# Performance work log

Hardware: AMD Instinct MI355X
Metric: run time of the kernel (lower is better)

Reference implementation:

```python
import jax, jax.numpy as jnp
import numpy as np

B, Q, T, C = 2, 300, 25, 256
NH, NL, NP = 8, 4, 4
DFF = 1024
HD = C // NH
SHAPES = [(128, 128), (64, 64), (32, 32), (16, 16)]  # (H_l, W_l) per level
S = sum(h * w for h, w in SHAPES)
LQ = Q * T


def setup_inputs() -> dict:
    key = jax.random.key(0)
    ks = jax.random.split(key, 16)
    rn = lambda k, shape, s=0.02: jax.random.normal(k, shape, jnp.float32) * s
    starts = np.cumsum([0] + [h * w for h, w in SHAPES[:-1]])
    return {
        "tgt_text": jax.random.normal(ks[0], (B, Q, T, C), jnp.float32),
        "query_pos_text": jax.random.normal(ks[1], (B, Q, T, C), jnp.float32),
        "reference_points": jax.random.uniform(ks[2], (B, LQ, NL, 2), jnp.float32),
        "src": jax.random.normal(ks[3], (B, S, C), jnp.float32),
        "src_spatial_shapes": jnp.array(SHAPES, jnp.int32),
        "level_start_index": jnp.array(starts, jnp.int32),
        "in_proj_w": rn(ks[4], (3 * C, C)), "in_proj_b": jnp.zeros((3 * C,), jnp.float32),
        "out_proj_w": rn(ks[5], (C, C)), "out_proj_b": jnp.zeros((C,), jnp.float32),
        "ln1_g": jnp.ones((C,), jnp.float32), "ln1_b": jnp.zeros((C,), jnp.float32),
        "samp_off_w": rn(ks[6], (NH * NL * NP * 2, C)), "samp_off_b": rn(ks[7], (NH * NL * NP * 2,), 0.5),
        "aw_w": rn(ks[8], (NH * NL * NP, C)), "aw_b": jnp.zeros((NH * NL * NP,), jnp.float32),
        "vp_w": rn(ks[9], (C, C)), "vp_b": jnp.zeros((C,), jnp.float32),
        "op_w": rn(ks[10], (C, C)), "op_b": jnp.zeros((C,), jnp.float32),
        "ln2_g": jnp.ones((C,), jnp.float32), "ln2_b": jnp.zeros((C,), jnp.float32),
        "ffn1_w": rn(ks[11], (DFF, C)), "ffn1_b": jnp.zeros((DFF,), jnp.float32),
        "ffn2_w": rn(ks[12], (C, DFF)), "ffn2_b": jnp.zeros((C,), jnp.float32),
        "ln3_g": jnp.ones((C,), jnp.float32), "ln3_b": jnp.zeros((C,), jnp.float32),
    }


def _ln(x, g, b):
    m = jnp.mean(x, axis=-1, keepdims=True)
    v = jnp.var(x, axis=-1, keepdims=True)
    return (x - m) / jnp.sqrt(v + 1e-5) * g + b


def _self_attn(tgt, pos, in_proj_w, in_proj_b, out_proj_w, out_proj_b):
    # torch nn.MultiheadAttention math: q,k carry pos, v is raw tgt
    qk = (tgt + pos).reshape(B * Q, T, C)
    x = tgt.reshape(B * Q, T, C)
    Wq, Wk, Wv = jnp.split(in_proj_w, 3, axis=0)
    bq, bk, bv = jnp.split(in_proj_b, 3, axis=0)
    heads = lambda t: t.reshape(B * Q, T, NH, HD).transpose(0, 2, 1, 3)
    q = heads(qk @ Wq.T + bq)
    k = heads(qk @ Wk.T + bk)
    v = heads(x @ Wv.T + bv)
    attn = jax.nn.softmax(jnp.einsum("bhqd,bhkd->bhqk", q, k) / jnp.sqrt(jnp.float32(HD)), axis=-1)
    o = jnp.einsum("bhqk,bhkd->bhqd", attn, v).transpose(0, 2, 1, 3).reshape(B * Q, T, C)
    return (o @ out_proj_w.T + out_proj_b).reshape(B, Q, T, C)


def _ms_deform_attn(query, reference_points, src, shapes, samp_off_w, samp_off_b, aw_w, aw_b, vp_w, vp_b, op_w, op_b):
    # query: [B, LQ, C]; src: [B, S, C]
    value = (src @ vp_w.T + vp_b).reshape(B, S, NH, HD)
    off = (query @ samp_off_w.T + samp_off_b).reshape(B, LQ, NH, NL, NP, 2)
    aw = jax.nn.softmax((query @ aw_w.T + aw_b).reshape(B, LQ, NH, NL * NP), axis=-1)
    aw = aw.reshape(B, LQ, NH, NL, NP)
    # normalizer is (W_l, H_l)
    norm = jnp.array([[w, h] for (h, w) in shapes], jnp.float32)
    loc = reference_points[:, :, None, :, None, :] + off / norm[None, None, None, :, None, :]
    starts = np.cumsum([0] + [h * w for h, w in shapes])
    accum = jnp.zeros((B, NH, LQ, HD), jnp.float32)
    for l, (Hl, Wl) in enumerate(shapes):
        vl = value[:, starts[l]:starts[l] + Hl * Wl].transpose(0, 2, 1, 3)  # [B,NH,HW,HD]
        # grid_sample align_corners=False pixel coords
        xl = (loc[:, :, :, l, :, 0] * Wl - 0.5).transpose(0, 2, 1, 3).reshape(B, NH, LQ * NP)
        yl = (loc[:, :, :, l, :, 1] * Hl - 0.5).transpose(0, 2, 1, 3).reshape(B, NH, LQ * NP)
        x0 = jnp.floor(xl); y0 = jnp.floor(yl)
        wx1 = xl - x0; wy1 = yl - y0
        x0i = x0.astype(jnp.int32); y0i = y0.astype(jnp.int32)
        samp = jnp.zeros((B, NH, LQ * NP, HD), jnp.float32)
        for dx, dy, w in ((0, 0, (1 - wx1) * (1 - wy1)), (1, 0, wx1 * (1 - wy1)),
                          (0, 1, (1 - wx1) * wy1), (1, 1, wx1 * wy1)):
            xi = x0i + dx; yi = y0i + dy
            valid = (xi >= 0) & (xi < Wl) & (yi >= 0) & (yi < Hl)
            lin = jnp.clip(yi, 0, Hl - 1) * Wl + jnp.clip(xi, 0, Wl - 1)
            g = jnp.take_along_axis(vl, lin[..., None], axis=2)  # [B,NH,LQ*NP,HD]
            samp = samp + g * (w * valid)[..., None]
        samp = samp.reshape(B, NH, LQ, NP, HD)
        awl = aw[:, :, :, l, :].transpose(0, 2, 1, 3)  # [B,NH,LQ,NP]
        accum = accum + jnp.sum(samp * awl[..., None], axis=3)
    out = accum.transpose(0, 2, 1, 3).reshape(B, LQ, C)
    return out @ op_w.T + op_b


def reference(tgt_text, query_pos_text, reference_points, src, src_spatial_shapes, level_start_index,
              in_proj_w, in_proj_b, out_proj_w, out_proj_b, ln1_g, ln1_b,
              samp_off_w, samp_off_b, aw_w, aw_b, vp_w, vp_b, op_w, op_b, ln2_g, ln2_b,
              ffn1_w, ffn1_b, ffn2_w, ffn2_b, ln3_g, ln3_b):
    shapes = [tuple(int(v) for v in row) for row in np.asarray(src_spatial_shapes)]  # static
    # --- intra-text self-attention ---
    tgt2 = _self_attn(tgt_text, query_pos_text, in_proj_w, in_proj_b, out_proj_w, out_proj_b)
    tgt = _ln(tgt_text + tgt2, ln1_g, ln1_b)
    # --- multi-scale deformable cross-attention ---
    query = (tgt + query_pos_text).reshape(B, LQ, C)
    cross = _ms_deform_attn(query, reference_points, src, shapes,
                            samp_off_w, samp_off_b, aw_w, aw_b, vp_w, vp_b, op_w, op_b)
    tgt = _ln(tgt + cross.reshape(B, Q, T, C), ln2_g, ln2_b)
    # --- FFN ---
    ffn = jax.nn.relu(tgt @ ffn1_w.T + ffn1_b) @ ffn2_w.T + ffn2_b
    return _ln(tgt + ffn, ln3_g, ln3_b)
```

## Files before the change

kernel.cpp:

```cpp
#include <hip/hip_runtime.h>
#include <cstddef>

#define B_ 2
#define Q_ 300
#define T_ 25
#define C_ 256
#define NH_ 8
#define NL_ 4
#define NP_ 4
#define HD_ 32
#define DFF_ 1024
#define LQ_ (Q_ * T_)
#define NTOK_ (B_ * LQ_)
#define S_ 21760
#define BS_ (B_ * S_)

typedef __bf16 bf16x8 __attribute__((ext_vector_type(8)));
typedef float floatx4 __attribute__((ext_vector_type(4)));
typedef unsigned short ushort_t;

__device__ __forceinline__ unsigned pack_bf16(float x, float y) {
    unsigned ux = __float_as_uint(x) + 0x8000u;
    unsigned uy = __float_as_uint(y) + 0x8000u;
    return (ux >> 16) | (uy & 0xFFFF0000u);
}
__device__ __forceinline__ ushort_t f2bf_s(float x) {
    return (ushort_t)((__float_as_uint(x) + 0x8000u) >> 16);
}
__device__ __forceinline__ float bf2f(ushort_t u) {
    return __uint_as_float((unsigned)u << 16);
}

#define GBN 128
#define GBK 32
#define LDA_S 40

template<int AMODE, int OUT_BF16, int GBMT>
__global__ __launch_bounds__(256) void gemm_t(
    const void* __restrict__ Av, const float* __restrict__ A2,
    const float* __restrict__ W, const float* __restrict__ W2, int N1,
    const float* __restrict__ bias, const float* __restrict__ bias2,
    void* __restrict__ Cv, long long partStride,
    int M, int N, int K, int kChunk, int ldc, int relu)
{
    constexpr int LA = GBMT / 32;
    constexpr int WM = GBMT / 2;
    constexpr int NI = WM / 16;

    __shared__ unsigned short Asl[GBMT * LDA_S];
    __shared__ unsigned short Bsl[GBN * LDA_S];

    const int m0 = blockIdx.x * GBMT;
    const int n0 = blockIdx.y * GBN;
    const int z  = blockIdx.z;
    const int kbeg = z * kChunk;
    const int kend = min(K, kbeg + kChunk);

    const int t  = threadIdx.x;
    const int wid  = t >> 6;
    const int lane = t & 63;
    const int wm = (wid >> 1) * WM;
    const int wn = (wid & 1) * 64;
    const int fm = lane & 15;
    const int fq = (lane >> 4) * 8;

    floatx4 acc[NI][4];
    #pragma unroll
    for (int i = 0; i < NI; ++i)
        #pragma unroll
        for (int j = 0; j < 4; ++j)
            acc[i][j] = (floatx4){0.f, 0.f, 0.f, 0.f};

    float4 pa[LA];
    uint2  pab[LA];
    float4 pw[4];
    const float* Af = (const float*)Av;
    const ushort_t* Ab = (const ushort_t*)Av;

    auto load_tiles = [&](int k0) {
        #pragma unroll
        for (int i = 0; i < LA; ++i) {
            int idx = t + 256 * i;
            int row = idx >> 3;
            int c4  = (idx & 7) * 4;
            int gm = m0 + row;
            if constexpr (AMODE == 2) {
                uint2 v = {0u, 0u};
                if (gm < M) v = *(const uint2*)(Ab + (size_t)gm * K + k0 + c4);
                pab[i] = v;
            } else {
                float4 v = make_float4(0.f, 0.f, 0.f, 0.f);
                if (gm < M) {
                    v = *(const float4*)(Af + (size_t)gm * K + k0 + c4);
                    if constexpr (AMODE == 1) {
                        float4 v2 = *(const float4*)(A2 + (size_t)gm * K + k0 + c4);
                        v.x += v2.x; v.y += v2.y; v.z += v2.z; v.w += v2.w;
                    }
                }
                pa[i] = v;
            }
        }
        #pragma unroll
        for (int i = 0; i < 4; ++i) {
            int idx = t + 256 * i;
            int row = idx >> 3;
            int c4  = (idx & 7) * 4;
            int gn = n0 + row;
            const float* wr;
            if (W2 && gn >= N1) wr = W2 + (size_t)(gn - N1) * K;
            else                wr = W + (size_t)gn * K;
            pw[i] = *(const float4*)(wr + k0 + c4);
        }
    };

    load_tiles(kbeg);
    for (int k0 = kbeg; k0 < kend; k0 += GBK) {
        #pragma unroll
        for (int i = 0; i < LA; ++i) {
            int idx = t + 256 * i;
            int row = idx >> 3;
            int c4  = (idx & 7) * 4;
            if constexpr (AMODE == 2) {
                *(uint2*)&Asl[row * LDA_S + c4] = pab[i];
            } else {
                uint2 p;
                p.x = pack_bf16(pa[i].x, pa[i].y);
                p.y = pack_bf16(pa[i].z, pa[i].w);
                *(uint2*)&Asl[row * LDA_S + c4] = p;
            }
        }
        #pragma unroll
        for (int i = 0; i < 4; ++i) {
            int idx = t + 256 * i;
            int row = idx >> 3;
            int c4  = (idx & 7) * 4;
            uint2 q;
            q.x = pack_bf16(pw[i].x, pw[i].y);
            q.y = pack_bf16(pw[i].z, pw[i].w);
            *(uint2*)&Bsl[row * LDA_S + c4] = q;
        }
        __syncthreads();

        if (k0 + GBK < kend) load_tiles(k0 + GBK);

        bf16x8 af[NI], bfr[4];
        #pragma unroll
        for (int i = 0; i < NI; ++i)
            af[i] = *(const bf16x8*)&Asl[(wm + i * 16 + fm) * LDA_S + fq];
        #pragma unroll
        for (int j = 0; j < 4; ++j)
            bfr[j] = *(const bf16x8*)&Bsl[(wn + j * 16 + fm) * LDA_S + fq];

        #pragma unroll
        for (int i = 0; i < NI; ++i)
            #pragma unroll
            for (int j = 0; j < 4; ++j)
                acc[i][j] = __builtin_amdgcn_mfma_f32_16x16x32_bf16(af[i], bfr[j], acc[i][j], 0, 0, 0);
        __syncthreads();
    }

    float* Cf = (float*)Cv + (long long)z * partStride;
    ushort_t* Cb = (ushort_t*)Cv;
    const int cr = (lane >> 4) * 4;
    const int cc = lane & 15;
    #pragma unroll
    for (int j = 0; j < 4; ++j) {
        int gn = n0 + wn + j * 16 + cc;
        float bia = 0.f;
        if (z == 0) bia = (bias2 && gn >= N1) ? bias2[gn - N1] : bias[gn];
        #pragma unroll
        for (int i = 0; i < NI; ++i) {
            #pragma unroll
            for (int r = 0; r < 4; ++r) {
                int gm = m0 + wm + i * 16 + cr + r;
                if (gm < M) {
                    float v = acc[i][j][r] + bia;
                    if (relu) v = fmaxf(v, 0.f);
                    if constexpr (OUT_BF16) Cb[(size_t)gm * ldc + gn] = f2bf_s(v);
                    else                    Cf[(size_t)gm * ldc + gn] = v;
                }
            }
        }
    }
}

__global__ __launch_bounds__(64) void attn_kernel(
    const ushort_t* __restrict__ qkv,
    ushort_t* __restrict__ o)
{
    int sh = blockIdx.x;
    int s = sh >> 3, h = sh & 7;
    __shared__ float qs[T_][HD_], ks[T_][HD_], vs[T_][HD_];
    int t = threadIdx.x;

    for (int idx = t; idx < T_ * HD_; idx += 64) {
        int i = idx >> 5, d = idx & 31;
        size_t base = ((size_t)(s * T_ + i)) * 768 + h * HD_ + d;
        qs[i][d] = bf2f(qkv[base]);
        ks[i][d] = bf2f(qkv[base + 256]);
        vs[i][d] = bf2f(qkv[base + 512]);
    }
    __syncthreads();

    if (t < T_) {
        float sc[T_];
        float mx = -1e30f;
        #pragma unroll
        for (int j = 0; j < T_; ++j) {
            float dot = 0.f;
            #pragma unroll
            for (int d = 0; d < HD_; ++d) dot += qs[t][d] * ks[j][d];
            sc[j] = dot * 0.17677669529663687f;
            mx = fmaxf(mx, sc[j]);
        }
        float sum = 0.f;
        #pragma unroll
        for (int j = 0; j < T_; ++j) { sc[j] = __expf(sc[j] - mx); sum += sc[j]; }
        float inv = 1.f / sum;
        float out[HD_];
        #pragma unroll
        for (int d = 0; d < HD_; ++d) out[d] = 0.f;
        for (int j = 0; j < T_; ++j) {
            float p = sc[j] * inv;
            #pragma unroll
            for (int d = 0; d < HD_; ++d) out[d] += p * vs[j][d];
        }
        size_t ob = ((size_t)(s * T_ + t)) * C_ + h * HD_;
        #pragma unroll
        for (int d = 0; d < HD_; ++d) o[ob + d] = f2bf_s(out[d]);
    }
}

__global__ __launch_bounds__(256) void ln_kernel(
    const float* __restrict__ x, const float* __restrict__ r,
    int nparts, long long rstride,
    const float* __restrict__ g, const float* __restrict__ b,
    float* __restrict__ out, const float* __restrict__ pos,
    float* __restrict__ qout)
{
    int tok = blockIdx.x;
    int t = threadIdx.x;
    size_t base = (size_t)tok * C_;
    float v = x[base + t];
    for (int p = 0; p < nparts; ++p)
        v += r[(long long)base + t + (long long)p * rstride];

    float s = v, ss = v * v;
    #pragma unroll
    for (int off = 32; off; off >>= 1) {
        s += __shfl_down(s, off);
        ss += __shfl_down(ss, off);
    }
    __shared__ float ws[4], wss[4];
    __shared__ float mean_s, rstd_s;
    int wid = t >> 6, lane = t & 63;
    if (lane == 0) { ws[wid] = s; wss[wid] = ss; }
    __syncthreads();
    if (t == 0) {
        float S = 0.f, SS = 0.f;
        #pragma unroll
        for (int i = 0; i < 4; ++i) { S += ws[i]; SS += wss[i]; }
        float m = S / 256.f;
        float var = SS / 256.f - m * m;
        mean_s = m;
        rstd_s = rsqrtf(var + 1e-5f);
    }
    __syncthreads();
    float y = (v - mean_s) * rstd_s * g[t] + b[t];
    out[base + t] = y;
    if (qout) qout[base + t] = y + pos[base + t];
}

__global__ __launch_bounds__(256) void deform_kernel(
    const ushort_t* __restrict__ value,
    const float* __restrict__ d12,
    const float* __restrict__ refpts,
    ushort_t* __restrict__ out)
{
    const int lane = threadIdx.x & 63;
    const int wave = threadIdx.x >> 6;
    const int half = lane >> 5;
    const int tok = blockIdx.x * 8 + wave * 2 + half;
    const int h  = (lane >> 2) & 7;
    const int d8 = (lane & 3) * 8;
    const int b = tok / LQ_;

    const float* awp = d12 + (size_t)tok * 384 + 256 + h * 16;
    float logit[16];
    float mx = -1e30f;
    #pragma unroll
    for (int i = 0; i < 16; ++i) { logit[i] = awp[i]; mx = fmaxf(mx, logit[i]); }
    float sum = 0.f;
    #pragma unroll
    for (int i = 0; i < 16; ++i) { logit[i] = __expf(logit[i] - mx); sum += logit[i]; }
    float inv = 1.f / sum;

    const float* offp = d12 + (size_t)tok * 384 + h * 32;
    const float* refp = refpts + (size_t)tok * (NL_ * 2);

    const int HW[4]     = {128, 64, 32, 16};
    const int starts[4] = {0, 16384, 20480, 21504};

    float accv[8];
    #pragma unroll
    for (int i = 0; i < 8; ++i) accv[i] = 0.f;

    #pragma unroll
    for (int l = 0; l < 4; ++l) {
        const int Hl = HW[l], Wl = HW[l];
        float rx = refp[l * 2 + 0], ry = refp[l * 2 + 1];
        const ushort_t* vbase = value + ((size_t)b * S_ + starts[l]) * (NH_ * HD_) + h * HD_ + d8;
        #pragma unroll
        for (int p = 0; p < 4; ++p) {
            float ox = offp[(l * 4 + p) * 2 + 0];
            float oy = offp[(l * 4 + p) * 2 + 1];
            float xl = rx * (float)Wl + ox - 0.5f;
            float yl = ry * (float)Hl + oy - 0.5f;
            float x0f = floorf(xl), y0f = floorf(yl);
            int x0 = (int)x0f, y0 = (int)y0f;
            float wx1 = xl - x0f, wy1 = yl - y0f;
            float wx0 = 1.f - wx1, wy0 = 1.f - wy1;
            float aww = logit[l * 4 + p] * inv;

            #pragma unroll
            for (int c = 0; c < 4; ++c) {
                int dx = c & 1, dy = c >> 1;
                int xi = x0 + dx, yi = y0 + dy;
                float w = (dx ? wx1 : wx0) * (dy ? wy1 : wy0);
                bool valid = (xi >= 0) & (xi < Wl) & (yi >= 0) & (yi < Hl);
                int xc = min(max(xi, 0), Wl - 1);
                int yc = min(max(yi, 0), Hl - 1);
                float wc = (valid ? w : 0.f) * aww;
                uint4 raw = *(const uint4*)(vbase + ((size_t)(yc * Wl + xc)) * (NH_ * HD_));
                accv[0] += __uint_as_float((raw.x & 0xFFFFu) << 16) * wc;
                accv[1] += __uint_as_float(raw.x & 0xFFFF0000u) * wc;
                accv[2] += __uint_as_float((raw.y & 0xFFFFu) << 16) * wc;
                accv[3] += __uint_as_float(raw.y & 0xFFFF0000u) * wc;
                accv[4] += __uint_as_float((raw.z & 0xFFFFu) << 16) * wc;
                accv[5] += __uint_as_float(raw.z & 0xFFFF0000u) * wc;
                accv[6] += __uint_as_float((raw.w & 0xFFFFu) << 16) * wc;
                accv[7] += __uint_as_float(raw.w & 0xFFFF0000u) * wc;
            }
        }
    }
    uint4 po;
    po.x = pack_bf16(accv[0], accv[1]);
    po.y = pack_bf16(accv[2], accv[3]);
    po.z = pack_bf16(accv[4], accv[5]);
    po.w = pack_bf16(accv[6], accv[7]);
    *(uint4*)(out + (size_t)tok * C_ + h * HD_ + d8) = po;
}

extern "C" void kernel_launch(void* const* d_in, const int* in_sizes, int n_in,
                              void* d_out, int out_size, void* d_ws, size_t ws_size,
                              hipStream_t stream) {
    const float* tgt_text = (const float*)d_in[0];
    const float* pos      = (const float*)d_in[1];
    const float* refpts   = (const float*)d_in[2];
    const float* src      = (const float*)d_in[3];
    const float* in_proj_w  = (const float*)d_in[6];
    const float* in_proj_b  = (const float*)d_in[7];
    const float* out_proj_w = (const float*)d_in[8];
    const float* out_proj_b = (const float*)d_in[9];
    const float* ln1_g = (const float*)d_in[10];
    const float* ln1_b = (const float*)d_in[11];
    const float* samp_off_w = (const float*)d_in[12];
    const float* samp_off_b = (const float*)d_in[13];
    const float* aw_w = (const float*)d_in[14];
    const float* aw_b = (const float*)d_in[15];
    const float* vp_w = (const float*)d_in[16];
    const float* vp_b = (const float*)d_in[17];
    const float* op_w = (const float*)d_in[18];
    const float* op_b = (const float*)d_in[19];
    const float* ln2_g = (const float*)d_in[20];
    const float* ln2_b = (const float*)d_in[21];
    const float* ffn1_w = (const float*)d_in[22];
    const float* ffn1_b = (const float*)d_in[23];
    const float* ffn2_w = (const float*)d_in[24];
    const float* ffn2_b = (const float*)d_in[25];
    const float* ln3_g = (const float*)d_in[26];
    const float* ln3_b = (const float*)d_in[27];

    const long long NC = (long long)NTOK_ * C_;
    float* ws = (float*)d_ws;
    float* A    = ws;
    float* Bq   = ws + NC;
    float* Creg = ws + 2 * NC;
    float* D12  = Creg + (long long)NTOK_ * DFF_;
    float* E    = D12 + (long long)NTOK_ * 384;
    float* F    = E + NC;

    const int MB64  = (NTOK_ + 63) / 64;
    const int MB128 = (NTOK_ + 127) / 128;
    const int MBV64 = BS_ / 64;

    gemm_t<1, 1, 64><<<dim3(MB64, 4, 1), 256, 0, stream>>>(tgt_text, pos, in_proj_w, nullptr, 0,
        in_proj_b, nullptr, Creg, 0, NTOK_, 512, 256, 256, 768, 0);
    gemm_t<0, 1, 64><<<dim3(MB64, 2, 1), 256, 0, stream>>>(tgt_text, nullptr, in_proj_w + 512 * 256, nullptr, 0,
        in_proj_b + 512, nullptr, (void*)((ushort_t*)Creg + 512), 0, NTOK_, 256, 256, 256, 768, 0);
    attn_kernel<<<B_ * Q_ * NH_, 64, 0, stream>>>((const ushort_t*)Creg, (ushort_t*)E);
    gemm_t<2, 0, 64><<<dim3(MB64, 2, 1), 256, 0, stream>>>(E, nullptr, out_proj_w, nullptr, 0,
        out_proj_b, nullptr, F, 0, NTOK_, 256, 256, 256, 256, 0);
    ln_kernel<<<NTOK_, 256, 0, stream>>>(tgt_text, F, 1, 0,
                                         ln1_g, ln1_b, A, pos, Bq);
    gemm_t<0, 1, 64><<<dim3(MBV64, 2, 1), 256, 0, stream>>>(src, nullptr, vp_w, nullptr, 0,
        vp_b, nullptr, Creg, 0, BS_, 256, 256, 256, 256, 0);
    gemm_t<0, 0, 64><<<dim3(MB64, 3, 1), 256, 0, stream>>>(Bq, nullptr, samp_off_w, aw_w, 256,
        samp_off_b, aw_b, D12, 0, NTOK_, 384, 256, 256, 384, 0);
    deform_kernel<<<NTOK_ / 8, 256, 0, stream>>>((const ushort_t*)Creg, D12, refpts, (ushort_t*)E);
    gemm_t<2, 0, 64><<<dim3(MB64, 2, 1), 256, 0, stream>>>(E, nullptr, op_w, nullptr, 0,
        op_b, nullptr, F, 0, NTOK_, 256, 256, 256, 256, 0);
    ln_kernel<<<NTOK_, 256, 0, stream>>>(A, F, 1, 0,
                                         ln2_g, ln2_b, A, nullptr, nullptr);
    gemm_t<0, 1, 128><<<dim3(MB128, 8, 1), 256, 0, stream>>>(A, nullptr, ffn1_w, nullptr, 0,
        ffn1_b, nullptr, Creg, 0, NTOK_, DFF_, 256, 256, DFF_, 1);
    gemm_t<2, 0, 64><<<dim3(MB64, 2, 2), 256, 0, stream>>>(Creg, nullptr, ffn2_w, nullptr, 0,
        ffn2_b, nullptr, E, NC, NTOK_, 256, 1024, 512, 256, 0);
    ln_kernel<<<NTOK_, 256, 0, stream>>>(A, E, 2, NC,
                                         ln3_g, ln3_b, (float*)d_out, nullptr, nullptr);
}
```

Measured before the change: 454.4 us.

## Fuse QKV and value-projection GEMMs, head-major value layout, wave-per-token LayerNorm

Merges the Q/K, V and value-projection GEMMs into one launch that writes bf16 output. The value projection is stored head-major as [B][head][S][32], so each deformable-attention bilinear gather reads a contiguous 64-byte row per pixel. LayerNorm is rewritten so each wave handles one token with float4 loads and shuffle reductions, removing shared-memory syncs. The aim is to cut launch count, improve gather locality and raise LN memory throughput, at the cost of a scattered store in the value-GEMM epilogue.

```diff
diff --git a/kernel.cpp b/kernel.cpp
--- a/kernel.cpp
+++ b/kernel.cpp
@@ -184,6 +184,138 @@
     }
 }
 
+__global__ __launch_bounds__(256) void gemm3(
+    const float* __restrict__ tgt, const float* __restrict__ pos,
+    const float* __restrict__ src,
+    const float* __restrict__ ipw, const float* __restrict__ ipb,
+    const float* __restrict__ vpw, const float* __restrict__ vpb,
+    ushort_t* __restrict__ qkv, ushort_t* __restrict__ valt)
+{
+    __shared__ unsigned short Asl[64 * LDA_S];
+    __shared__ unsigned short Bsl[GBN * LDA_S];
+
+    int g = blockIdx.x;
+    const float *A, *A2, *W, *bias;
+    int m0, n0, M, vt;
+    ushort_t* C;
+    if (g < 940)       { A = tgt; A2 = pos;     W = ipw;             bias = ipb;
+                         m0 = (g >> 2) * 64; n0 = (g & 3) * 128; M = NTOK_; vt = 0; C = qkv; }
+    else if (g < 1410) { g -= 940; A = tgt; A2 = nullptr; W = ipw + 512 * 256; bias = ipb + 512;
+                         m0 = (g >> 1) * 64; n0 = (g & 1) * 128; M = NTOK_; vt = 0; C = qkv + 512; }
+    else               { g -= 1410; A = src; A2 = nullptr; W = vpw;  bias = vpb;
+                         m0 = (g >> 1) * 64; n0 = (g & 1) * 128; M = BS_; vt = 1; C = valt; }
+    const int K = 256;
+
+    const int t  = threadIdx.x;
+    const int wid  = t >> 6;
+    const int lane = t & 63;
+    const int wm = (wid >> 1) * 32;
+    const int wn = (wid & 1) * 64;
+    const int fm = lane & 15;
+    const int fq = (lane >> 4) * 8;
+
+    floatx4 acc[2][4];
+    #pragma unroll
+    for (int i = 0; i < 2; ++i)
+        #pragma unroll
+        for (int j = 0; j < 4; ++j)
+            acc[i][j] = (floatx4){0.f, 0.f, 0.f, 0.f};
+
+    float4 pa[2], pw[4];
+    auto load_tiles = [&](int k0) {
+        #pragma unroll
+        for (int i = 0; i < 2; ++i) {
+            int idx = t + 256 * i;
+            int row = idx >> 3;
+            int c4  = (idx & 7) * 4;
+            int gm = m0 + row;
+            float4 v = make_float4(0.f, 0.f, 0.f, 0.f);
+            if (gm < M) {
+                v = *(const float4*)(A + (size_t)gm * K + k0 + c4);
+                if (A2) {
+                    float4 v2 = *(const float4*)(A2 + (size_t)gm * K + k0 + c4);
+                    v.x += v2.x; v.y += v2.y; v.z += v2.z; v.w += v2.w;
+                }
+            }
+            pa[i] = v;
+        }
+        #pragma unroll
+        for (int i = 0; i < 4; ++i) {
+            int idx = t + 256 * i;
+            int row = idx >> 3;
+            int c4  = (idx & 7) * 4;
+            pw[i] = *(const float4*)(W + (size_t)(n0 + row) * K + k0 + c4);
+        }
+    };
+
+    load_tiles(0);
+    for (int k0 = 0; k0 < K; k0 += GBK) {
+        #pragma unroll
+        for (int i = 0; i < 2; ++i) {
+            int idx = t + 256 * i;
+            int row = idx >> 3;
+            int c4  = (idx & 7) * 4;
+            uint2 p;
+            p.x = pack_bf16(pa[i].x, pa[i].y);
+            p.y = pack_bf16(pa[i].z, pa[i].w);
+            *(uint2*)&Asl[row * LDA_S + c4] = p;
+        }
+        #pragma unroll
+        for (int i = 0; i < 4; ++i) {
+            int idx = t + 256 * i;
+            int row = idx >> 3;
+            int c4  = (idx & 7) * 4;
+            uint2 q;
+            q.x = pack_bf16(pw[i].x, pw[i].y);
+            q.y = pack_bf16(pw[i].z, pw[i].w);
+            *(uint2*)&Bsl[row * LDA_S + c4] = q;
+        }
+        __syncthreads();
+
+        if (k0 + GBK < K) load_tiles(k0 + GBK);
+
+        bf16x8 af[2], bfr[4];
+        #pragma unroll
+        for (int i = 0; i < 2; ++i)
+            af[i] = *(const bf16x8*)&Asl[(wm + i * 16 + fm) * LDA_S + fq];
+        #pragma unroll
+        for (int j = 0; j < 4; ++j)
+            bfr[j] = *(const bf16x8*)&Bsl[(wn + j * 16 + fm) * LDA_S + fq];
+
+        #pragma unroll
+        for (int i = 0; i < 2; ++i)
+            #pragma unroll
+            for (int j = 0; j < 4; ++j)
+                acc[i][j] = __builtin_amdgcn_mfma_f32_16x16x32_bf16(af[i], bfr[j], acc[i][j], 0, 0, 0);
+        __syncthreads();
+    }
+
+    const int cr = (lane >> 4) * 4;
+    const int cc = lane & 15;
+    #pragma unroll
+    for (int j = 0; j < 4; ++j) {
+        int gn = n0 + wn + j * 16 + cc;
+        float bia = bias[gn];
+        #pragma unroll
+        for (int i = 0; i < 2; ++i) {
+            #pragma unroll
+            for (int r = 0; r < 4; ++r) {
+                int gm = m0 + wm + i * 16 + cr + r;
+                if (gm < M) {
+                    ushort_t o = f2bf_s(acc[i][j][r] + bia);
+                    if (vt) {
+                        int bb = gm >= S_;
+                        int s  = gm - bb * S_;
+                        C[(((size_t)(bb * 8 + (gn >> 5))) * S_ + s) * 32 + (gn & 31)] = o;
+                    } else {
+                        C[(size_t)gm * 768 + gn] = o;
+                    }
+                }
+            }
+        }
+    }
+}
+
 __global__ __launch_bounds__(64) void attn_kernel(
     const ushort_t* __restrict__ qkv,
     ushort_t* __restrict__ o)
@@ -231,44 +363,48 @@
     }
 }
 
-__global__ __launch_bounds__(256) void ln_kernel(
+__global__ __launch_bounds__(256) void ln4_kernel(
     const float* __restrict__ x, const float* __restrict__ r,
     int nparts, long long rstride,
     const float* __restrict__ g, const float* __restrict__ b,
     float* __restrict__ out, const float* __restrict__ pos,
     float* __restrict__ qout)
 {
-    int tok = blockIdx.x;
-    int t = threadIdx.x;
-    size_t base = (size_t)tok * C_;
-    float v = x[base + t];
-    for (int p = 0; p < nparts; ++p)
-        v += r[(long long)base + t + (long long)p * rstride];
-
-    float s = v, ss = v * v;
-    #pragma unroll
-    for (int off = 32; off; off >>= 1) {
-        s += __shfl_down(s, off);
-        ss += __shfl_down(ss, off);
-    }
-    __shared__ float ws[4], wss[4];
-    __shared__ float mean_s, rstd_s;
-    int wid = t >> 6, lane = t & 63;
-    if (lane == 0) { ws[wid] = s; wss[wid] = ss; }
-    __syncthreads();
-    if (t == 0) {
-        float S = 0.f, SS = 0.f;
-        #pragma unroll
-        for (int i = 0; i < 4; ++i) { S += ws[i]; SS += wss[i]; }
-        float m = S / 256.f;
-        float var = SS / 256.f - m * m;
-        mean_s = m;
-        rstd_s = rsqrtf(var + 1e-5f);
-    }
-    __syncthreads();
-    float y = (v - mean_s) * rstd_s * g[t] + b[t];
-    out[base + t] = y;
-    if (qout) qout[base + t] = y + pos[base + t];
+    const int wave = threadIdx.x >> 6;
+    const int lane = threadIdx.x & 63;
+    const int tok = blockIdx.x * 4 + wave;
+    const size_t base = (size_t)tok * C_ + lane * 4;
+
+    float4 v = *(const float4*)(x + base);
+    for (int p = 0; p < nparts; ++p) {
+        float4 rv = *(const float4*)(r + base + (long long)p * rstride);
+        v.x += rv.x; v.y += rv.y; v.z += rv.z; v.w += rv.w;
+    }
+    float s  = v.x + v.y + v.z + v.w;
+    float ss = v.x * v.x + v.y * v.y + v.z * v.z + v.w * v.w;
+    #pragma unroll
+    for (int m = 32; m; m >>= 1) {
+        s  += __shfl_xor(s, m);
+        ss += __shfl_xor(ss, m);
+    }
+    float mean = s * (1.f / 256.f);
+    float var  = ss * (1.f / 256.f) - mean * mean;
+    float rstd = rsqrtf(var + 1e-5f);
+
+    float4 gv = *(const float4*)(g + lane * 4);
+    float4 bv = *(const float4*)(b + lane * 4);
+    float4 y;
+    y.x = (v.x - mean) * rstd * gv.x + bv.x;
+    y.y = (v.y - mean) * rstd * gv.y + bv.y;
+    y.z = (v.z - mean) * rstd * gv.z + bv.z;
+    y.w = (v.w - mean) * rstd * gv.w + bv.w;
+    *(float4*)(out + base) = y;
+    if (qout) {
+        float4 pv = *(const float4*)(pos + base);
+        float4 q;
+        q.x = y.x + pv.x; q.y = y.y + pv.y; q.z = y.z + pv.z; q.w = y.w + pv.w;
+        *(float4*)(qout + base) = q;
+    }
 }
 
 __global__ __launch_bounds__(256) void deform_kernel(
@@ -309,7 +445,7 @@
     for (int l = 0; l < 4; ++l) {
         const int Hl = HW[l], Wl = HW[l];
         float rx = refp[l * 2 + 0], ry = refp[l * 2 + 1];
-        const ushort_t* vbase = value + ((size_t)b * S_ + starts[l]) * (NH_ * HD_) + h * HD_ + d8;
+        const ushort_t* vbase = value + (((size_t)(b * 8 + h)) * S_ + starts[l]) * HD_ + d8;
         #pragma unroll
         for (int p = 0; p < 4; ++p) {
             float ox = offp[(l * 4 + p) * 2 + 0];
@@ -331,7 +467,7 @@
                 int xc = min(max(xi, 0), Wl - 1);
                 int yc = min(max(yi, 0), Hl - 1);
                 float wc = (valid ? w : 0.f) * aww;
-                uint4 raw = *(const uint4*)(vbase + ((size_t)(yc * Wl + xc)) * (NH_ * HD_));
+                uint4 raw = *(const uint4*)(vbase + (size_t)(yc * Wl + xc) * HD_);
                 accv[0] += __uint_as_float((raw.x & 0xFFFFu) << 16) * wc;
                 accv[1] += __uint_as_float(raw.x & 0xFFFF0000u) * wc;
                 accv[2] += __uint_as_float((raw.y & 0xFFFFu) << 16) * wc;
@@ -390,32 +526,30 @@
     float* E    = D12 + (long long)NTOK_ * 384;
     float* F    = E + NC;
 
+    ushort_t* qkv  = (ushort_t*)Creg;
+    ushort_t* valt = (ushort_t*)Creg + (size_t)NTOK_ * 768;
+
     const int MB64  = (NTOK_ + 63) / 64;
     const int MB128 = (NTOK_ + 127) / 128;
-    const int MBV64 = BS_ / 64;
-
-    gemm_t<1, 1, 64><<<dim3(MB64, 4, 1), 256, 0, stream>>>(tgt_text, pos, in_proj_w, nullptr, 0,
-        in_proj_b, nullptr, Creg, 0, NTOK_, 512, 256, 256, 768, 0);
-    gemm_t<0, 1, 64><<<dim3(MB64, 2, 1), 256, 0, stream>>>(tgt_text, nullptr, in_proj_w + 512 * 256, nullptr, 0,
-        in_proj_b + 512, nullptr, (void*)((ushort_t*)Creg + 512), 0, NTOK_, 256, 256, 256, 768, 0);
-    attn_kernel<<<B_ * Q_ * NH_, 64, 0, stream>>>((const ushort_t*)Creg, (ushort_t*)E);
+
+    gemm3<<<2770, 256, 0, stream>>>(tgt_text, pos, src, in_proj_w, in_proj_b,
+                                    vp_w, vp_b, qkv, valt);
+    attn_kernel<<<B_ * Q_ * NH_, 64, 0, stream>>>(qkv, (ushort_t*)E);
     gemm_t<2, 0, 64><<<dim3(MB64, 2, 1), 256, 0, stream>>>(E, nullptr, out_proj_w, nullptr, 0,
         out_proj_b, nullptr, F, 0, NTOK_, 256, 256, 256, 256, 0);
-    ln_kernel<<<NTOK_, 256, 0, stream>>>(tgt_text, F, 1, 0,
-                                         ln1_g, ln1_b, A, pos, Bq);
-    gemm_t<0, 1, 64><<<dim3(MBV64, 2, 1), 256, 0, stream>>>(src, nullptr, vp_w, nullptr, 0,
-        vp_b, nullptr, Creg, 0, BS_, 256, 256, 256, 256, 0);
+    ln4_kernel<<<NTOK_ / 4, 256, 0, stream>>>(tgt_text, F, 1, 0,
+                                              ln1_g, ln1_b, A, pos, Bq);
     gemm_t<0, 0, 64><<<dim3(MB64, 3, 1), 256, 0, stream>>>(Bq, nullptr, samp_off_w, aw_w, 256,
         samp_off_b, aw_b, D12, 0, NTOK_, 384, 256, 256, 384, 0);
-    deform_kernel<<<NTOK_ / 8, 256, 0, stream>>>((const ushort_t*)Creg, D12, refpts, (ushort_t*)E);
+    deform_kernel<<<NTOK_ / 8, 256, 0, stream>>>(valt, D12, refpts, (ushort_t*)E);
     gemm_t<2, 0, 64><<<dim3(MB64, 2, 1), 256, 0, stream>>>(E, nullptr, op_w, nullptr, 0,
         op_b, nullptr, F, 0, NTOK_, 256, 256, 256, 256, 0);
-    ln_kernel<<<NTOK_, 256, 0, stream>>>(A, F, 1, 0,
-                                         ln2_g, ln2_b, A, nullptr, nullptr);
+    ln4_kernel<<<NTOK_ / 4, 256, 0, stream>>>(A, F, 1, 0,
+                                              ln2_g, ln2_b, A, nullptr, nullptr);
     gemm_t<0, 1, 128><<<dim3(MB128, 8, 1), 256, 0, stream>>>(A, nullptr, ffn1_w, nullptr, 0,
         ffn1_b, nullptr, Creg, 0, NTOK_, DFF_, 256, 256, DFF_, 1);
     gemm_t<2, 0, 64><<<dim3(MB64, 2, 2), 256, 0, stream>>>(Creg, nullptr, ffn2_w, nullptr, 0,
         ffn2_b, nullptr, E, NC, NTOK_, 256, 1024, 512, 256, 0);
-    ln_kernel<<<NTOK_, 256, 0, stream>>>(A, E, 2, NC,
-                                         ln3_g, ln3_b, (float*)d_out, nullptr, nullptr);
-}
+    ln4_kernel<<<NTOK_ / 4, 256, 0, stream>>>(A, E, 2, NC,
+                                              ln3_g, ln3_b, (float*)d_out, nullptr, nullptr);
+}
```

After: 457.2 us. About the same (+0.6%).
